# Performance work log

Measured on AMD Instinct MI355X. Metric: run time of the kernel, lower is better.

Reference implementation:

```python
import jax, jax.numpy as jnp
import numpy as np
from jax import lax

IN_CH, FEAT, EMB, P = 384, 256, 32, 64
OUT_CH = (256, 512, 1024, 1024)
EPS_BN = 1e-5


def _conv(x, w, b, stride=1, pad=1, groups=1):
    # x: (B,C,H,W), w: (O, C//groups, kh, kw) torch OIHW layout
    y = lax.conv_general_dilated(x, w, (stride, stride), ((pad, pad), (pad, pad)),
                                 dimension_numbers=('NCHW', 'OIHW', 'NCHW'),
                                 feature_group_count=groups)
    return y + b[None, :, None, None]


def _bn(x, g, b, m, v):
    scale = (g / jnp.sqrt(v + EPS_BN))[None, :, None, None]
    return (x - m[None, :, None, None]) * scale + b[None, :, None, None]


def _convT_block(x, w, b, k):
    # ConvTranspose2d with kernel_size == stride == k, padding 0 (non-overlapping)
    # w: (C_in, C_out, k, k) torch layout
    B, C, H, W = x.shape
    O = w.shape[1]
    y = jnp.einsum('bchw,coij->bohiwj', x, w).reshape(B, O, H * k, W * k)
    return y + b[None, :, None, None]


def _resize_ac(x, oh, ow):
    # bilinear interpolation, align_corners=True; x: (B,C,H,W)
    H, W = x.shape[-2], x.shape[-1]
    def idx(n_in, n_out):
        c = jnp.arange(n_out, dtype=x.dtype) * ((n_in - 1) / max(n_out - 1, 1))
        i0 = jnp.clip(jnp.floor(c).astype(jnp.int32), 0, max(n_in - 2, 0))
        return i0, c - i0.astype(x.dtype)
    if oh != H:
        i0, t = idx(H, oh)
        x = x[:, :, i0, :] * (1.0 - t)[:, None] + x[:, :, jnp.minimum(i0 + 1, H - 1), :] * t[:, None]
    if ow != W:
        j0, t = idx(W, ow)
        x = x[:, :, :, j0] * (1.0 - t) + x[:, :, :, jnp.minimum(j0 + 1, W - 1)] * t
    return x


def _avg3(x):
    # F.avg_pool2d(k=3, s=1, p=1) with count_include_pad=True -> always /9
    s = lax.reduce_window(x, jnp.float32(0.0), lax.add, (1, 1, 3, 3), (1, 1, 1, 1),
                          ((0, 0), (0, 0), (1, 1), (1, 1)))
    return s / 9.0


def _forward(tokens0, tokens1, tokens2, tokens3,
             proj_w0, proj_b0, proj_w1, proj_b1, proj_w2, proj_b2, proj_w3, proj_b3,
             up_w0, up_b0, up_w1, up_b1, down_w3, down_b3,
             fuse_w, fuse_b,
             pe_w1, pe_b1, pe_bn_g, pe_bn_b, pe_bn_m, pe_bn_v, pe_w2, pe_b2,
             prototypes, prototype_biases, bias_scale,
             smooth_w, smooth_b,
             head_w1, head_b1, hbn1_g, hbn1_b, hbn1_m, hbn1_v,
             head_w2, head_b2, hbn2_g, hbn2_b, hbn2_m, hbn2_v,
             head_w3, head_b3, residual_scale,
             patch_h, patch_w):
    B = tokens0.shape[0]
    toks = (tokens0, tokens1, tokens2, tokens3)
    proj = ((proj_w0, proj_b0), (proj_w1, proj_b1), (proj_w2, proj_b2), (proj_w3, proj_b3))
    feats = []
    for t, (w, b) in zip(toks, proj):
        x = t.transpose(0, 2, 1).reshape(B, t.shape[-1], patch_h, patch_w)
        x = jnp.einsum('bchw,oc->bohw', x, w[:, :, 0, 0]) + b[None, :, None, None]  # 1x1 proj
        feats.append(x)
    f0 = _convT_block(feats[0], up_w0, up_b0, 4)
    f1 = _convT_block(feats[1], up_w1, up_b1, 2)
    f2 = feats[2]                                         # identity
    f3 = _conv(feats[3], down_w3, down_b3, stride=2)
    th, tw = f0.shape[-2], f0.shape[-1]
    fused = jnp.concatenate([f0, _resize_ac(f1, th, tw), _resize_ac(f2, th, tw), _resize_ac(f3, th, tw)], axis=1)
    path1 = jax.nn.relu(jnp.einsum('bchw,oc->bohw', fused, fuse_w[:, :, 0, 0]) + fuse_b[None, :, None, None])
    H, W = patch_h * 14, patch_w * 14
    path1 = _resize_ac(path1, H, W)
    pe = _conv(path1, pe_w1, pe_b1)
    pe = jax.nn.relu(_bn(pe, pe_bn_g, pe_bn_b, pe_bn_m, pe_bn_v))
    pe = _conv(pe, pe_w2, pe_b2)                          # (B, EMB, H, W)
    sim = jnp.einsum('behw,pe->bphw', pe, prototypes) / jnp.sqrt(jnp.float32(pe.shape[1]))
    # edge map from embedding gradients, replicate-padded
    gx = jnp.abs(pe[:, :, :, :-1] - pe[:, :, :, 1:])
    gy = jnp.abs(pe[:, :, :-1, :] - pe[:, :, 1:, :])
    gx = jnp.concatenate([gx, gx[:, :, :, -1:]], axis=3)
    gy = jnp.concatenate([gy, gy[:, :, -1:, :]], axis=2)
    edge = (gx.mean(axis=1, keepdims=True) + gy.mean(axis=1, keepdims=True)) * 0.5
    mask = (edge > edge.mean()).astype(pe.dtype)
    for _ in range(2):  # fixed 2-step edge-aware smoothing
        sim = mask * sim + (1.0 - mask) * _avg3(sim)
    # first softmax over prototypes -> entropy regularizer
    act1 = jax.nn.softmax(sim, axis=1)
    activation_entropy = -(act1 * jnp.log(act1 + 1e-8)).sum(axis=1).mean()
    # spatial smoothing conv then second softmax over prototypes
    sim = _conv(sim, smooth_w, smooth_b)
    act = jax.nn.softmax(sim, axis=1)                     # (B, P, H, W)
    bb = 1.0 + jnp.tanh(prototype_biases) * bias_scale    # (P,)
    base_biases = jnp.broadcast_to(bb[None, :], (B, bb.shape[0]))
    base_gain = jnp.einsum('bphw,p->bhw', act, bb)[:, None]  # (B,1,H,W)
    # 64 per-prototype residual heads == grouped convs with groups=P
    n_proto = act.shape[1]
    h = jax.nn.relu(_bn(_conv(act, head_w1, head_b1, groups=n_proto), hbn1_g, hbn1_b, hbn1_m, hbn1_v))
    h = jax.nn.relu(_bn(_conv(h, head_w2, head_b2, groups=n_proto), hbn2_g, hbn2_b, hbn2_m, hbn2_v))
    res = _conv(h, head_w3, head_b3, groups=n_proto)      # (B, P, H, W)
    weighted = (act * res).sum(axis=1, keepdims=True)
    gain = base_gain * (1.0 + jnp.tanh(weighted) * residual_scale)
    instance_bias_map = jnp.clip(gain, 0.5, 2.0)
    return instance_bias_map, act, base_biases, weighted, pe, activation_entropy


def setup_inputs() -> dict:
    key = jax.random.key(0)
    B, N, PH, PW = 2, 256, 16, 16
    ks = iter(jax.random.split(key, 48))
    def rnd(shape, s=1.0):
        return jax.random.normal(next(ks), shape, dtype=jnp.float32) * s
    inp = {}
    for i in range(4):
        inp['tokens%d' % i] = rnd((B, N, IN_CH))
    for i, oc in enumerate(OUT_CH):
        inp['proj_w%d' % i] = rnd((oc, IN_CH, 1, 1), 0.02)
        inp['proj_b%d' % i] = rnd((oc,), 0.01)
    inp['up_w0'] = rnd((OUT_CH[0], OUT_CH[0], 4, 4), 0.02)
    inp['up_b0'] = rnd((OUT_CH[0],), 0.01)
    inp['up_w1'] = rnd((OUT_CH[1], OUT_CH[1], 2, 2), 0.02)
    inp['up_b1'] = rnd((OUT_CH[1],), 0.01)
    inp['down_w3'] = rnd((OUT_CH[3], OUT_CH[3], 3, 3), 0.01)
    inp['down_b3'] = rnd((OUT_CH[3],), 0.01)
    inp['fuse_w'] = rnd((FEAT, sum(OUT_CH), 1, 1), 0.01)
    inp['fuse_b'] = rnd((FEAT,), 0.01)
    inp['pe_w1'] = rnd((FEAT // 2, FEAT, 3, 3), 0.02)
    inp['pe_b1'] = rnd((FEAT // 2,), 0.01)
    inp['pe_bn_g'] = 1.0 + rnd((FEAT // 2,), 0.1)
    inp['pe_bn_b'] = rnd((FEAT // 2,), 0.01)
    inp['pe_bn_m'] = rnd((FEAT // 2,), 0.01)
    inp['pe_bn_v'] = jnp.ones((FEAT // 2,), jnp.float32)
    inp['pe_w2'] = rnd((EMB, FEAT // 2, 3, 3), 0.02)
    inp['pe_b2'] = rnd((EMB,), 0.01)
    inp['prototypes'] = rnd((P, EMB), 0.01)
    inp['prototype_biases'] = rnd((P,), 0.1)
    inp['bias_scale'] = jnp.asarray(0.2, jnp.float32)
    inp['smooth_w'] = rnd((P, P, 3, 3), 0.02)
    inp['smooth_b'] = rnd((P,), 0.01)
    inp['head_w1'] = rnd((P * 8, 1, 3, 3), 0.1)
    inp['head_b1'] = rnd((P * 8,), 0.01)
    inp['hbn1_g'] = 1.0 + rnd((P * 8,), 0.1)
    inp['hbn1_b'] = rnd((P * 8,), 0.01)
    inp['hbn1_m'] = rnd((P * 8,), 0.01)
    inp['hbn1_v'] = jnp.ones((P * 8,), jnp.float32)
    inp['head_w2'] = rnd((P * 8, 8, 3, 3), 0.1)
    inp['head_b2'] = rnd((P * 8,), 0.01)
    inp['hbn2_g'] = 1.0 + rnd((P * 8,), 0.1)
    inp['hbn2_b'] = rnd((P * 8,), 0.01)
    inp['hbn2_m'] = rnd((P * 8,), 0.01)
    inp['hbn2_v'] = jnp.ones((P * 8,), jnp.float32)
    inp['head_w3'] = rnd((P, 8, 3, 3), 0.1)
    inp['head_b3'] = rnd((P,), 0.01)
    inp['residual_scale'] = jnp.asarray(0.1, jnp.float32)
    inp['patch_h'] = PH
    inp['patch_w'] = PW
    return inp


def reference(tokens0, tokens1, tokens2, tokens3,
              proj_w0, proj_b0, proj_w1, proj_b1, proj_w2, proj_b2, proj_w3, proj_b3,
              up_w0, up_b0, up_w1, up_b1, down_w3, down_b3,
              fuse_w, fuse_b,
              pe_w1, pe_b1, pe_bn_g, pe_bn_b, pe_bn_m, pe_bn_v, pe_w2, pe_b2,
              prototypes, prototype_biases, bias_scale,
              smooth_w, smooth_b,
              head_w1, head_b1, hbn1_g, hbn1_b, hbn1_m, hbn1_v,
              head_w2, head_b2, hbn2_g, hbn2_b, hbn2_m, hbn2_v,
              head_w3, head_b3, residual_scale,
              patch_h, patch_w):
    return _forward(tokens0, tokens1, tokens2, tokens3,
                    proj_w0, proj_b0, proj_w1, proj_b1, proj_w2, proj_b2, proj_w3, proj_b3,
                    up_w0, up_b0, up_w1, up_b1, down_w3, down_b3,
                    fuse_w, fuse_b,
                    pe_w1, pe_b1, pe_bn_g, pe_bn_b, pe_bn_m, pe_bn_v, pe_w2, pe_b2,
                    prototypes, prototype_biases, bias_scale,
                    smooth_w, smooth_b,
                    head_w1, head_b1, hbn1_g, hbn1_b, hbn1_m, hbn1_v,
                    head_w2, head_b2, hbn2_g, hbn2_b, hbn2_m, hbn2_v,
                    head_w3, head_b3, residual_scale,
                    patch_h, patch_w)
```

## Files before the change

kernel.cpp:

```cpp
#include <hip/hip_runtime.h>
#include <math.h>

#define BATCH 2
#define NTOK 256
#define INCH 384
#define NP 50176
#define HW 224
#define NPROTO 64
#define EMBD 32

#define OFF_FEATS0   0u
#define OFF_FEATS1   131072u
#define OFF_FEATS2   393216u
#define OFF_FEATS3   917504u
#define OFF_TOKT     1441792u
#define OFF_F0       2228224u
#define OFF_F1       4325376u
#define OFF_F3       5373952u
#define OFF_FUSEDBF  5505024u
#define OFF_WD       5505024u
#define OFF_PART     14942208u
#define OFF_P64C     28573696u
#define OFF_P224C    0u
#define OFF_T1       25690112u
#define OFF_SIMA     0u
#define OFF_SIMB     6422528u
#define OFF_EDGE     12845056u
#define OFF_RES      13000000u
#define OFF_WB       13000000u
#define OFF_SHIFT    13200000u
#define OFF_BGAIN    19422528u
#define OFF_BB       19522880u
#define OFF_ACC      19523008u
#define OFF_WF       19523072u
#define OFF_WFUSE    20000000u
#define OFF_WCV0     20500000u
#define OFF_WCV1     21600000u
#define OFF_WC2      22700000u
#define OFF_WSM      22750000u

#define O_IBM 0u
#define O_ACT 100352u
#define O_BB  6522880u
#define O_WT  6523008u
#define O_PE  6623360u
#define O_ENT 9834624u

typedef __attribute__((ext_vector_type(8))) short bf16x8;
typedef __attribute__((ext_vector_type(4))) float f32x4;
typedef __attribute__((ext_vector_type(2))) float f32x2;

__device__ __forceinline__ short f2bf(float f) {
    unsigned u = __float_as_uint(f);
    unsigned r = (u + 0x7fffu + ((u >> 16) & 1u)) >> 16;
    return (short)r;
}
__device__ __forceinline__ float bf2f(short s) {
    return __uint_as_float(((unsigned)(unsigned short)s) << 16);
}

__global__ void k_transpose(const float* __restrict__ in, float* __restrict__ out) {
    int idx = blockIdx.x * 256 + threadIdx.x;
    int n = idx & 255;
    int c = (idx >> 8) % INCH;
    int b = idx / (INCH * NTOK);
    out[idx] = in[(size_t)b * INCH * NTOK + (size_t)n * INCH + c];
}

__global__ __launch_bounds__(256) void k_proj(const float* __restrict__ A,
                                              const float* __restrict__ W,
                                              const float* __restrict__ bias,
                                              float* __restrict__ out, int O) {
    int p = threadIdx.x;
    int o = blockIdx.x, b = blockIdx.y;
    const float* a = A + (size_t)b * INCH * NTOK + p;
    const float* w = W + (size_t)o * INCH;
    float acc = bias[o];
    for (int c = 0; c < INCH; ++c) acc = fmaf(a[(size_t)c * NTOK], w[c], acc);
    out[((size_t)b * O + o) * NTOK + p] = acc;
}

template <int NT>
__global__ __launch_bounds__(256) void k_wcvprep(const float* __restrict__ W,
                                                 float* __restrict__ WP, int C, int M) {
    __shared__ float t[32][33];
    int c0 = blockIdx.x * 32, m0 = blockIdx.y * 32;
    int tx = threadIdx.x & 31, ty = threadIdx.x >> 5;
#pragma unroll
    for (int r = 0; r < 4; ++r) {
        int cl = ty + r * 8;
        t[cl][tx] = W[(size_t)(c0 + cl) * M + m0 + tx];
    }
    __syncthreads();
    for (int i = threadIdx.x; i < 1024; i += 256) {
        int ml = i % NT;
        int tmp = i / NT;
        int cl = tmp & 31;
        int mh = tmp >> 5;
        WP[(size_t)(m0 / NT + mh) * C * NT + (size_t)(c0 + cl) * NT + ml] = t[cl][mh * NT + ml];
    }
}

template <int NT, int CCH, int K>
__global__ __launch_bounds__(256) void k_convt2(const float* __restrict__ X,
                                                const float* __restrict__ WP,
                                                const float* __restrict__ bias,
                                                float* __restrict__ out,
                                                int C, int O) {
    __shared__ float sX[CCH * 256];
    int tid = threadIdx.x;
    int nt = blockIdx.x, b = blockIdx.y;
    float acc[NT];
#pragma unroll
    for (int j = 0; j < NT; ++j) acc[j] = 0.f;
    const float* Xb = X + (size_t)b * C * 256;
    for (int cc = 0; cc < C; cc += CCH) {
        __syncthreads();
        const f32x4* Xg4 = (const f32x4*)(Xb + (size_t)cc * 256);
        f32x4* s4 = (f32x4*)sX;
        for (int i = tid; i < CCH * 64; i += 256) s4[i] = Xg4[i];
        __syncthreads();
        const float* wr = WP + ((size_t)nt * C + cc) * NT;
        for (int c = 0; c < CCH; ++c) {
            float xv = sX[c * 256 + tid];
            const float* w = wr + c * NT;
#pragma unroll
            for (int j = 0; j < NT; ++j) acc[j] = fmaf(xv, w[j], acc[j]);
        }
    }
    int h = tid >> 4, w = tid & 15;
    int S = 16 * K;
#pragma unroll
    for (int j = 0; j < NT; ++j) {
        int m = nt * NT + j;
        int o = m / (K * K);
        int ij = m - o * (K * K);
        int ii = ij / K, jj = ij - ii * K;
        out[((size_t)b * O + o) * (size_t)(S * S) + (h * K + ii) * S + (w * K + jj)] =
            acc[j] + bias[o];
    }
}

__global__ __launch_bounds__(256) void k_wdprep(const float* __restrict__ W,
                                                float* __restrict__ WP) {
    __shared__ float t[32][33];
    int k0 = blockIdx.x * 32, o0 = blockIdx.y * 32;
    int tx = threadIdx.x & 31, ty = threadIdx.x >> 5;
#pragma unroll
    for (int r = 0; r < 4; ++r) {
        int orow = ty + r * 8;
        t[orow][tx] = W[(size_t)(o0 + orow) * 9216 + k0 + tx];
    }
    __syncthreads();
#pragma unroll
    for (int r = 0; r < 4; ++r) {
        int krow = ty + r * 8;
        int o = o0 + tx;
        WP[(size_t)(o >> 6) * 589824 + (size_t)(k0 + krow) * 64 + (o & 63)] = t[tx][krow];
    }
}

__global__ __launch_bounds__(256) void k_down2(const float* __restrict__ X,
                                               const float* __restrict__ WP,
                                               float* __restrict__ part) {
    __shared__ float sX[64 * 256];
    int tid = threadIdx.x;
    int ot = blockIdx.x, kc = blockIdx.y, b = blockIdx.z;
    int c0 = kc * 64;
    const float* Xg = X + ((size_t)b * 1024 + c0) * 256;
    for (int i = tid; i < 16384; i += 256) {
        int c = i >> 8, px = i & 255;
        int sy = px >> 4, sx = px & 15;
        int par = (sy & 1) * 2 + (sx & 1);
        sX[(c * 4 + par) * 64 + (sy >> 1) * 8 + (sx >> 1)] = Xg[i];
    }
    __syncthreads();
    int lane = tid & 63;
    int w = __builtin_amdgcn_readfirstlane(tid >> 6);
    int oh = lane >> 3, ow = lane & 7;
    int loff[9]; float lmsk[9];
#pragma unroll
    for (int kh = 0; kh < 3; ++kh)
#pragma unroll
        for (int kw = 0; kw < 3; ++kw) {
            int py = (kh == 1) ? 0 : 1;
            int pxp = (kw == 1) ? 0 : 1;
            int u = oh - ((kh == 0) ? 1 : 0);
            int v = ow - ((kw == 0) ? 1 : 0);
            float m = (u >= 0 && v >= 0) ? 1.f : 0.f;
            if (u < 0) u = 0;
            if (v < 0) v = 0;
            loff[kh * 3 + kw] = (py * 2 + pxp) * 64 + u * 8 + v;
            lmsk[kh * 3 + kw] = m;
        }
    float acc[16];
#pragma unroll
    for (int j = 0; j < 16; ++j) acc[j] = 0.f;
    const float* wb = WP + (size_t)ot * 589824 + (size_t)c0 * 576 + w * 16;
    for (int c = 0; c < 64; ++c) {
        const float* xb = sX + c * 256;
        const float* wc = wb + (size_t)c * 576;
#pragma unroll
        for (int tap = 0; tap < 9; ++tap) {
            float xv = xb[loff[tap]] * lmsk[tap];
            const float* wr = wc + tap * 64;
#pragma unroll
            for (int j = 0; j < 16; ++j) acc[j] = fmaf(xv, wr[j], acc[j]);
        }
    }
    float* pp = part + ((size_t)((kc * 2 + b) * 1024 + ot * 64 + w * 16)) * 64 + lane;
#pragma unroll
    for (int j = 0; j < 16; ++j) pp[(size_t)j * 64] = acc[j];
}

__global__ __launch_bounds__(256) void k_downred(const float* __restrict__ part,
                                                 const float* __restrict__ bias,
                                                 float* __restrict__ out) {
    int idx = blockIdx.x * 256 + threadIdx.x;
    int o = (idx >> 6) & 1023;
    int b = idx >> 16;
    int px = idx & 63;
    float s = bias[o];
#pragma unroll
    for (int kcs = 0; kcs < 16; ++kcs)
        s += part[((size_t)(kcs * 2 + b) * 1024 + o) * 64 + px];
    out[idx] = s;
}

__global__ void k_fusedcat_bf(const float* __restrict__ f0, const float* __restrict__ f1,
                              const float* __restrict__ f2, const float* __restrict__ f3,
                              short* __restrict__ out) {
    int idx = blockIdx.x * 256 + threadIdx.x;
    int ch = idx % 2816;
    int t = idx / 2816;
    int pos = t & 4095;
    int b = t >> 12;
    float v;
    if (ch < 256) {
        v = f0[((size_t)(b * 256 + ch)) * 4096 + pos];
    } else {
        const float* src; int sh;
        if (ch < 768)       { src = f1 + ((size_t)(b * 512 + (ch - 256))) * 1024; sh = 32; }
        else if (ch < 1792) { src = f2 + ((size_t)(b * 1024 + (ch - 768))) * 256; sh = 16; }
        else                { src = f3 + ((size_t)(b * 1024 + (ch - 1792))) * 64; sh = 8;  }
        int y = pos >> 6, x = pos & 63;
        float r = (float)(sh - 1) / 63.0f;
        float cy = y * r, cx = x * r;
        int i0 = (int)cy; if (i0 > sh - 2) i0 = sh - 2;
        int j0 = (int)cx; if (j0 > sh - 2) j0 = sh - 2;
        float ty = cy - (float)i0, tx = cx - (float)j0;
        const float* s0 = src + i0 * sh + j0;
        float v00 = s0[0], v01 = s0[1], v10 = s0[sh], v11 = s0[sh + 1];
        float c0 = v00 + ty * (v10 - v00);
        float c1 = v01 + ty * (v11 - v01);
        v = c0 + tx * (c1 - c0);
    }
    out[idx] = f2bf(v);
}

__global__ void k_wfuseprep(const float* __restrict__ w, short* __restrict__ wb) {
    int idx = blockIdx.x * 256 + threadIdx.x;
    int j = idx & 7;
    int lane = (idx >> 3) & 63;
    int ntile = (idx >> 9) & 15;
    int chunk = idx >> 13;
    int oc = ntile * 16 + (lane & 15);
    int c = chunk * 32 + (lane >> 4) * 8 + j;
    wb[idx] = f2bf(w[(size_t)oc * 2816 + c]);
}

__global__ __launch_bounds__(256) void k_fuse_mfma(const short* __restrict__ A,
                                                   const bf16x8* __restrict__ WB,
                                                   const float* __restrict__ bias,
                                                   short* __restrict__ out) {
    int tid = threadIdx.x;
    int lane = tid & 63, w = tid >> 6;
    int row0 = blockIdx.x * 16;
    int l15 = lane & 15, q = lane >> 4;
    int arow = row0 + l15;
    f32x4 acc[4];
#pragma unroll
    for (int nn = 0; nn < 4; ++nn) acc[nn] = (f32x4){0.f, 0.f, 0.f, 0.f};
    const short* arp = A + (size_t)arow * 2816 + q * 8;
    for (int chunk = 0; chunk < 88; ++chunk) {
        bf16x8 a = *(const bf16x8*)(arp + chunk * 32);
        const bf16x8* wbp = WB + ((size_t)(chunk * 16 + w * 4) * 64) + lane;
#pragma unroll
        for (int nn = 0; nn < 4; ++nn) {
            bf16x8 bf = wbp[nn * 64];
            acc[nn] = __builtin_amdgcn_mfma_f32_16x16x32_bf16(a, bf, acc[nn], 0, 0, 0);
        }
    }
#pragma unroll
    for (int nn = 0; nn < 4; ++nn) {
        int oc = (w * 4 + nn) * 16 + l15;
        float bs = bias[oc];
#pragma unroll
        for (int r = 0; r < 4; ++r) {
            int m = q * 4 + r;
            out[(size_t)(row0 + m) * 256 + oc] = f2bf(fmaxf(acc[nn][r] + bs, 0.f));
        }
    }
}

__global__ void k_resize224bf2(const short* __restrict__ in, short* __restrict__ out) {
    int idx = blockIdx.x * 256 + threadIdx.x;
    int c8 = (idx & 31) * 8;
    int p = idx >> 5;
    int b = p / NP;
    int pos = p - b * NP;
    int y = pos / HW, x = pos - y * HW;
    const float r = (float)(63.0 / 223.0);
    float cy = y * r, cx = x * r;
    int i0 = (int)cy; if (i0 > 62) i0 = 62;
    int j0 = (int)cx; if (j0 > 62) j0 = 62;
    float ty = cy - (float)i0, tx = cx - (float)j0;
    const short* base = in + ((size_t)b * 4096) * 256 + c8;
    const bf16x8 v00 = *(const bf16x8*)(base + (size_t)(i0 * 64 + j0) * 256);
    const bf16x8 v01 = *(const bf16x8*)(base + (size_t)(i0 * 64 + j0 + 1) * 256);
    const bf16x8 v10 = *(const bf16x8*)(base + (size_t)((i0 + 1) * 64 + j0) * 256);
    const bf16x8 v11 = *(const bf16x8*)(base + (size_t)((i0 + 1) * 64 + j0 + 1) * 256);
    bf16x8 o;
#pragma unroll
    for (int k = 0; k < 8; ++k) {
        float a00 = bf2f(v00[k]), a01 = bf2f(v01[k]);
        float a10 = bf2f(v10[k]), a11 = bf2f(v11[k]);
        float c0 = a00 + ty * (a10 - a00);
        float c1 = a01 + ty * (a11 - a01);
        o[k] = f2bf(c0 + tx * (c1 - c0));
    }
    *(bf16x8*)(out + ((size_t)b * NP + pos) * 256 + c8) = o;
}

__global__ void k_w1prep(const float* __restrict__ w, const float* __restrict__ bias,
                         const float* __restrict__ g, const float* __restrict__ bb,
                         const float* __restrict__ m, const float* __restrict__ v,
                         short* __restrict__ wb, float* __restrict__ shift) {
    int idx = blockIdx.x * 256 + threadIdx.x;
    int j = idx & 7;
    int lane = (idx >> 3) & 63;
    int nt = (idx >> 9) & 7;
    int tc = idx >> 12;
    int tap = tc % 9, chunk = tc / 9;
    int oc = nt * 16 + (lane & 15);
    int c = chunk * 32 + (lane >> 4) * 8 + j;
    float s = g[oc] * rsqrtf(v[oc] + 1e-5f);
    wb[idx] = f2bf(w[((size_t)oc * 256 + c) * 9 + tap] * s);
    if (idx < 128) {
        float si = g[idx] * rsqrtf(v[idx] + 1e-5f);
        shift[idx] = (bias[idx] - m[idx]) * si + bb[idx];
    }
}

__global__ __launch_bounds__(256) void k_conv1mfma(const short* __restrict__ X,
                                                   const bf16x8* __restrict__ WB,
                                                   const float* __restrict__ shift,
                                                   float* __restrict__ out) {
    int tid = threadIdx.x;
    int lane = tid & 63, w = tid >> 6;
    int t = blockIdx.x;
    int b = blockIdx.y;
    int ty0 = (t / 28) * 16, tx0 = (t % 28) * 8;
    int l15 = lane & 15, q = lane >> 4;
    int loc0 = w * 32 + l15;
    int loc1 = loc0 + 16;
    int py0 = ty0 + (loc0 >> 3), px0 = tx0 + (loc0 & 7);
    int py1 = ty0 + (loc1 >> 3), px1 = tx0 + (loc1 & 7);
    int csub = q * 8;
    f32x4 acc0[8], acc1[8];
#pragma unroll
    for (int nt = 0; nt < 8; ++nt) {
        acc0[nt] = (f32x4){0.f, 0.f, 0.f, 0.f};
        acc1[nt] = (f32x4){0.f, 0.f, 0.f, 0.f};
    }
    const short* Xb = X + (size_t)b * NP * 256;
    const bf16x8 zv = {0, 0, 0, 0, 0, 0, 0, 0};
    for (int chunk = 0; chunk < 8; ++chunk) {
        int c0 = chunk * 32 + csub;
#pragma unroll
        for (int tap = 0; tap < 9; ++tap) {
            int dy = tap / 3 - 1, dx = tap % 3 - 1;
            int sy0 = py0 + dy, sx0 = px0 + dx;
            int sy1 = py1 + dy, sx1 = px1 + dx;
            bf16x8 a0 = zv, a1 = zv;
            if ((unsigned)sy0 < HW && (unsigned)sx0 < HW)
                a0 = *(const bf16x8*)(Xb + ((size_t)sy0 * HW + sx0) * 256 + c0);
            if ((unsigned)sy1 < HW && (unsigned)sx1 < HW)
                a1 = *(const bf16x8*)(Xb + ((size_t)sy1 * HW + sx1) * 256 + c0);
            const bf16x8* wbp = WB + (size_t)((chunk * 9 + tap) * 8) * 64 + lane;
#pragma unroll
            for (int nt = 0; nt < 8; ++nt) {
                bf16x8 bf = wbp[nt * 64];
                acc0[nt] = __builtin_amdgcn_mfma_f32_16x16x32_bf16(a0, bf, acc0[nt], 0, 0, 0);
                acc1[nt] = __builtin_amdgcn_mfma_f32_16x16x32_bf16(a1, bf, acc1[nt], 0, 0, 0);
            }
        }
    }
    int m0 = w * 32, m1 = w * 32 + 16;
#pragma unroll
    for (int nt = 0; nt < 8; ++nt) {
        int oc = nt * 16 + l15;
        float sh = shift[oc];
        float* ob = out + ((size_t)(b * 128 + oc)) * NP;
#pragma unroll
        for (int r = 0; r < 4; ++r) {
            int md = q * 4 + r;
            int lm = m0 + md;
            int py = ty0 + (lm >> 3), px = tx0 + (lm & 7);
            ob[py * HW + px] = fmaxf(acc0[nt][r] + sh, 0.f);
            lm = m1 + md;
            py = ty0 + (lm >> 3); px = tx0 + (lm & 7);
            ob[py * HW + px] = fmaxf(acc1[nt][r] + sh, 0.f);
        }
    }
}

__global__ void k_wc3prep(const float* __restrict__ W, float* __restrict__ WP,
                          int C, int O) {
    int idx = blockIdx.x * 256 + threadIdx.x;
    if (idx >= C * 9 * O) return;
    int o = idx % O;
    int t = idx / O;
    int tap = t % 9, c = t / 9;
    WP[idx] = W[((size_t)o * C + c) * 9 + tap];
}

template <int O, int C, int CCH>
__global__ __launch_bounds__(256) void k_conv3v2(const float* __restrict__ in,
                                                 const float* __restrict__ WP,
                                                 const float* __restrict__ bias,
                                                 float* __restrict__ out) {
    __shared__ float sX[CCH * 324];
    int tid = threadIdx.x;
    int tb = blockIdx.x, b = blockIdx.y;
    int ty0 = (tb / 14) * 16, tx0 = (tb % 14) * 16;
    int px = tid & 15, py = tid >> 4;
    float acc[O];
#pragma unroll
    for (int o = 0; o < O; ++o) acc[o] = 0.f;
    const float* ic = in + (size_t)b * C * NP;
    for (int cc = 0; cc < C; cc += CCH) {
        __syncthreads();
        for (int i = tid; i < CCH * 324; i += 256) {
            int c = i / 324;
            int r = i - c * 324;
            int y = r / 18, x = r - y * 18;
            int sy = ty0 + y - 1, sx = tx0 + x - 1;
            float v = 0.f;
            if ((unsigned)sy < HW && (unsigned)sx < HW)
                v = ic[(size_t)(cc + c) * NP + sy * HW + sx];
            sX[i] = v;
        }
        __syncthreads();
        const float* wr = WP + (size_t)cc * 9 * O;
        const float* xb = sX + py * 18 + px;
#pragma unroll 1
        for (int c = 0; c < CCH; ++c) {
            const float* xc = xb + c * 324;
            const float* wc = wr + (size_t)c * 9 * O;
#pragma unroll
            for (int kh = 0; kh < 3; ++kh)
#pragma unroll
                for (int kw = 0; kw < 3; ++kw) {
                    float xv = xc[kh * 18 + kw];
                    const float* wt = wc + (kh * 3 + kw) * O;
#pragma unroll
                    for (int o = 0; o < O; ++o) acc[o] = fmaf(xv, wt[o], acc[o]);
                }
        }
    }
    int gy = ty0 + py, gx = tx0 + px;
    float* ob = out + (size_t)b * O * NP + (size_t)gy * HW + gx;
#pragma unroll
    for (int o = 0; o < O; ++o) ob[(size_t)o * NP] = acc[o] + bias[o];
}

__global__ __launch_bounds__(256) void k_sim(const float* __restrict__ pe,
                                             const float* __restrict__ proto,
                                             float* __restrict__ sim) {
    int idx = blockIdx.x * 256 + threadIdx.x;
    int b = idx / NP, pos = idx - b * NP;
    const float* p = pe + (size_t)b * EMBD * NP + pos;
    float v[EMBD];
#pragma unroll
    for (int e = 0; e < EMBD; ++e) v[e] = p[(size_t)e * NP];
    const float scale = 1.0f / sqrtf(32.0f);
    float* so = sim + (size_t)b * NPROTO * NP + pos;
    for (int q = 0; q < NPROTO; ++q) {
        float acc = 0.f;
#pragma unroll
        for (int e = 0; e < EMBD; ++e) acc = fmaf(v[e], proto[q * EMBD + e], acc);
        so[(size_t)q * NP] = acc * scale;
    }
}

__global__ void k_init(float* acc) { if (threadIdx.x < 8) acc[threadIdx.x] = 0.f; }

__device__ __forceinline__ float block_reduce_sum(float v) {
    __shared__ float sh[4];
#pragma unroll
    for (int off = 32; off > 0; off >>= 1) v += __shfl_down(v, off);
    int lane = threadIdx.x & 63, wv = threadIdx.x >> 6;
    if (lane == 0) sh[wv] = v;
    __syncthreads();
    return (threadIdx.x == 0) ? (sh[0] + sh[1] + sh[2] + sh[3]) : 0.f;
}

__global__ __launch_bounds__(256) void k_edge(const float* __restrict__ pe,
                                              float* __restrict__ edge,
                                              float* __restrict__ acc) {
    int idx = blockIdx.x * 256 + threadIdx.x;
    int b = idx / NP, pos = idx - b * NP;
    int h = pos / HW, w = pos - h * HW;
    int wn = (w < HW - 1) ? w : HW - 2;
    int hn = (h < HW - 1) ? h : HW - 2;
    const float* pb = pe + (size_t)b * EMBD * NP;
    float sx = 0.f, sy = 0.f;
#pragma unroll 4
    for (int e = 0; e < EMBD; ++e) {
        const float* p = pb + (size_t)e * NP;
        sx += fabsf(p[h * HW + wn] - p[h * HW + wn + 1]);
        sy += fabsf(p[hn * HW + w] - p[hn * HW + HW + w]);
    }
    float ev = (sx + sy) * (0.5f / 32.0f);
    edge[idx] = ev;
    float tot = block_reduce_sum(ev);
    if (threadIdx.x == 0) atomicAdd(acc, tot);
}

__global__ void k_smooth(const float* __restrict__ sin_, const float* __restrict__ edge,
                         const float* __restrict__ acc, float* __restrict__ sout) {
    int idx = blockIdx.x * 256 + threadIdx.x;
    int pos = idx % NP;
    int bp = idx / NP;
    int b = bp >> 6;
    int h = pos / HW, w = pos - h * HW;
    float mean = acc[0] * (1.0f / 100352.0f);
    float m = (edge[(size_t)b * NP + pos] > mean) ? 1.f : 0.f;
    const float* sc = sin_ + (size_t)bp * NP;
    float s = 0.f;
#pragma unroll
    for (int dy = -1; dy <= 1; ++dy) {
        int yy = h + dy;
        if (yy < 0 || yy >= HW) continue;
#pragma unroll
        for (int dx = -1; dx <= 1; ++dx) {
            int xx = w + dx;
            if (xx < 0 || xx >= HW) continue;
            s += sc[yy * HW + xx];
        }
    }
    float c = sc[pos];
    sout[idx] = m * c + (1.f - m) * (s * (1.0f / 9.0f));
}

__global__ __launch_bounds__(256) void k_entropy(const float* __restrict__ sim,
                                                 float* __restrict__ acc) {
    int idx = blockIdx.x * 256 + threadIdx.x;
    int b = idx / NP, pos = idx - b * NP;
    const float* s = sim + (size_t)b * NPROTO * NP + pos;
    float v[NPROTO];
    float mx = -3.0e38f;
#pragma unroll
    for (int q = 0; q < NPROTO; ++q) { v[q] = s[(size_t)q * NP]; mx = fmaxf(mx, v[q]); }
    float sum = 0.f;
#pragma unroll
    for (int q = 0; q < NPROTO; ++q) { float e = expf(v[q] - mx); v[q] = e; sum += e; }
    float inv = 1.f / sum;
    float ent = 0.f;
#pragma unroll
    for (int q = 0; q < NPROTO; ++q) {
        float a = v[q] * inv;
        ent -= a * logf(a + 1e-8f);
    }
    float tot = block_reduce_sum(ent);
    if (threadIdx.x == 0) atomicAdd(acc + 1, tot);
}

__global__ void k_bb(const float* __restrict__ pb, const float* __restrict__ bs,
                     float* __restrict__ bbuf, float* __restrict__ obb) {
    int t = threadIdx.x;
    if (t < NPROTO) {
        float v = 1.f + tanhf(pb[t]) * bs[0];
        bbuf[t] = v;
        obb[t] = v;
        obb[NPROTO + t] = v;
    }
}

__global__ __launch_bounds__(256) void k_actsm(const float* __restrict__ sim,
                                               const float* __restrict__ bb,
                                               float* __restrict__ act,
                                               float* __restrict__ bgain) {
    int idx = blockIdx.x * 256 + threadIdx.x;
    int b = idx / NP, pos = idx - b * NP;
    const float* s = sim + (size_t)b * NPROTO * NP + pos;
    float v[NPROTO];
    float mx = -3.0e38f;
#pragma unroll
    for (int q = 0; q < NPROTO; ++q) { v[q] = s[(size_t)q * NP]; mx = fmaxf(mx, v[q]); }
    float sum = 0.f;
#pragma unroll
    for (int q = 0; q < NPROTO; ++q) { float e = expf(v[q] - mx); v[q] = e; sum += e; }
    float inv = 1.f / sum;
    float* a = act + (size_t)b * NPROTO * NP + pos;
    float bg = 0.f;
#pragma unroll
    for (int q = 0; q < NPROTO; ++q) {
        float p = v[q] * inv;
        a[(size_t)q * NP] = p;
        bg = fmaf(p, bb[q], bg);
    }
    bgain[idx] = bg;
}

__global__ void k_headprep(const float* __restrict__ w1, const float* __restrict__ b1,
                           const float* __restrict__ g1, const float* __restrict__ be1,
                           const float* __restrict__ m1, const float* __restrict__ v1,
                           const float* __restrict__ w2, const float* __restrict__ b2,
                           const float* __restrict__ g2, const float* __restrict__ be2,
                           const float* __restrict__ m2, const float* __restrict__ v2,
                           float* __restrict__ wf) {
    int oc = blockIdx.x * 256 + threadIdx.x;
    if (oc >= 512) return;
    float s1 = g1[oc] * rsqrtf(v1[oc] + 1e-5f);
#pragma unroll
    for (int k = 0; k < 9; ++k) wf[oc * 9 + k] = w1[oc * 9 + k] * s1;
    wf[41472 + oc] = (b1[oc] - m1[oc]) * s1 + be1[oc];
    float s2 = g2[oc] * rsqrtf(v2[oc] + 1e-5f);
    int g = oc >> 3, j = oc & 7;
#pragma unroll
    for (int icc = 0; icc < 8; ++icc)
#pragma unroll
        for (int k = 0; k < 9; ++k)
            wf[4608 + (size_t)g * 576 + icc * 72 + j * 9 + k] = w2[((size_t)oc * 8 + icc) * 9 + k] * s2;
    wf[41984 + oc] = (b2[oc] - m2[oc]) * s2 + be2[oc];
}

__global__ __launch_bounds__(256) void k_heads(
    const float* __restrict__ act, const float* __restrict__ wf,
    const float* __restrict__ w3, const float* __restrict__ b3,
    float* __restrict__ res) {
    __shared__ float sA[22 * 24];
    __shared__ float sH1[8][20 * 22];
    __shared__ float sH2[8][18 * 18];
    int tid = threadIdx.x;
    int tile = blockIdx.x, g = blockIdx.y, b = blockIdx.z;
    int oy0 = (tile / 14) * 16, ox0 = (tile % 14) * 16;
    const float* ain = act + (size_t)(b * NPROTO + g) * NP;

    for (int i = tid; i < 484; i += 256) {
        int y = i / 22, x = i - y * 22;
        int gy = oy0 - 3 + y, gx = ox0 - 3 + x;
        float v = 0.f;
        if ((unsigned)gy < HW && (unsigned)gx < HW) v = ain[gy * HW + gx];
        sA[y * 24 + x] = v;
    }
    __syncthreads();

    const float* b1f = wf + 41472 + g * 8;
    for (int i = tid; i < 400; i += 256) {
        int y = i / 20, x = i - y * 20;
        int gy = oy0 - 2 + y, gx = ox0 - 2 + x;
        float keep = ((unsigned)gy < HW && (unsigned)gx < HW) ? 1.f : 0.f;
        const float* s0 = sA + y * 24 + x;
        float r0 = s0[0],  r1 = s0[1],  r2 = s0[2];
        float r3 = s0[24], r4 = s0[25], r5 = s0[26];
        float r6 = s0[48], r7 = s0[49], r8 = s0[50];
#pragma unroll
        for (int j = 0; j < 8; ++j) {
            const float* w = wf + (g * 8 + j) * 9;
            float v = fmaf(r0, w[0], fmaf(r1, w[1], fmaf(r2, w[2],
                      fmaf(r3, w[3], fmaf(r4, w[4], fmaf(r5, w[5],
                      fmaf(r6, w[6], fmaf(r7, w[7], fmaf(r8, w[8], b1f[j])))))))));
            sH1[j][y * 22 + x] = fmaxf(v, 0.f) * keep;
        }
    }
    __syncthreads();

    const float* w2f = wf + 4608 + (size_t)g * 576;
    const float* b2f = wf + 41984 + g * 8;
    if (tid < 162) {
        int y2 = tid / 9, xp = (tid - y2 * 9) * 2;
        f32x2 a2[8];
#pragma unroll
        for (int j = 0; j < 8; ++j) { float bv = b2f[j]; a2[j] = (f32x2){bv, bv}; }
#pragma unroll
        for (int icc = 0; icc < 8; ++icc) {
            const float* s0 = &sH1[icc][y2 * 22 + xp];
            f32x2 t[9];
#pragma unroll
            for (int r = 0; r < 3; ++r) {
                float f0 = s0[r * 22], f1 = s0[r * 22 + 1];
                float f2 = s0[r * 22 + 2], f3 = s0[r * 22 + 3];
                t[r * 3 + 0] = (f32x2){f0, f1};
                t[r * 3 + 1] = (f32x2){f1, f2};
                t[r * 3 + 2] = (f32x2){f2, f3};
            }
            const float* wr = w2f + icc * 72;
#pragma unroll
            for (int j = 0; j < 8; ++j) {
                const float* wj = wr + j * 9;
#pragma unroll
                for (int k = 0; k < 9; ++k) {
                    float wv = wj[k];
                    a2[j] = __builtin_elementwise_fma(t[k], (f32x2){wv, wv}, a2[j]);
                }
            }
        }
        int gy = oy0 - 1 + y2;
        int gx0 = ox0 - 1 + xp;
        float k0 = ((unsigned)gy < HW && (unsigned)gx0 < HW) ? 1.f : 0.f;
        float k1 = ((unsigned)gy < HW && (unsigned)(gx0 + 1) < HW) ? 1.f : 0.f;
        f32x2 kp = (f32x2){k0, k1};
        const f32x2 z2 = (f32x2){0.f, 0.f};
#pragma unroll
        for (int j = 0; j < 8; ++j) {
            f32x2 v = __builtin_elementwise_max(a2[j], z2) * kp;
            sH2[j][y2 * 18 + xp] = v.x;
            sH2[j][y2 * 18 + xp + 1] = v.y;
        }
    }
    __syncthreads();

    if (tid < 128) {
        int y3 = tid >> 3, xp = (tid & 7) * 2;
        float bv = b3[g];
        f32x2 a2 = (f32x2){bv, bv};
#pragma unroll
        for (int icc = 0; icc < 8; ++icc) {
            const float* s0 = &sH2[icc][y3 * 18 + xp];
            const float* w = w3 + (size_t)(g * 8 + icc) * 9;
#pragma unroll
            for (int r = 0; r < 3; ++r) {
                float f0 = s0[r * 18], f1 = s0[r * 18 + 1];
                float f2 = s0[r * 18 + 2], f3 = s0[r * 18 + 3];
                float w0 = w[r * 3], w1 = w[r * 3 + 1], w2v = w[r * 3 + 2];
                a2 = __builtin_elementwise_fma((f32x2){f0, f1}, (f32x2){w0, w0}, a2);
                a2 = __builtin_elementwise_fma((f32x2){f1, f2}, (f32x2){w1, w1}, a2);
                a2 = __builtin_elementwise_fma((f32x2){f2, f3}, (f32x2){w2v, w2v}, a2);
            }
        }
        float* rp = res + (size_t)(b * NPROTO + g) * NP + (size_t)(oy0 + y3) * HW + (ox0 + xp);
        rp[0] = a2.x;
        rp[1] = a2.y;
    }
}

__global__ __launch_bounds__(256) void k_final(const float* __restrict__ act,
                                               const float* __restrict__ res,
                                               const float* __restrict__ bgain,
                                               const float* __restrict__ rscale,
                                               float* __restrict__ owt,
                                               float* __restrict__ oibm) {
    int idx = blockIdx.x * 256 + threadIdx.x;
    int b = idx / NP, pos = idx - b * NP;
    const float* a = act + (size_t)b * NPROTO * NP + pos;
    const float* r = res + (size_t)b * NPROTO * NP + pos;
    float wt = 0.f;
#pragma unroll
    for (int q = 0; q < NPROTO; ++q) wt = fmaf(a[(size_t)q * NP], r[(size_t)q * NP], wt);
    owt[idx] = wt;
    float gn = bgain[idx] * (1.f + tanhf(wt) * rscale[0]);
    gn = fminf(fmaxf(gn, 0.5f), 2.0f);
    oibm[idx] = gn;
}

__global__ void k_entfinal(const float* __restrict__ acc, float* __restrict__ o) {
    if (threadIdx.x == 0) o[0] = acc[1] * (1.0f / 100352.0f);
}

extern "C" void kernel_launch(void* const* d_in, const int* in_sizes, int n_in,
                              void* d_out, int out_size, void* d_ws, size_t ws_size,
                              hipStream_t stream) {
    const float* tokens[4] = {(const float*)d_in[0], (const float*)d_in[1],
                              (const float*)d_in[2], (const float*)d_in[3]};
    const float* proj_w[4] = {(const float*)d_in[4], (const float*)d_in[6],
                              (const float*)d_in[8], (const float*)d_in[10]};
    const float* proj_b[4] = {(const float*)d_in[5], (const float*)d_in[7],
                              (const float*)d_in[9], (const float*)d_in[11]};
    const float* up_w0 = (const float*)d_in[12]; const float* up_b0 = (const float*)d_in[13];
    const float* up_w1 = (const float*)d_in[14]; const float* up_b1 = (const float*)d_in[15];
    const float* down_w3 = (const float*)d_in[16]; const float* down_b3 = (const float*)d_in[17];
    const float* fuse_w = (const float*)d_in[18]; const float* fuse_b = (const float*)d_in[19];
    const float* pe_w1 = (const float*)d_in[20]; const float* pe_b1 = (const float*)d_in[21];
    const float* pe_bn_g = (const float*)d_in[22]; const float* pe_bn_b = (const float*)d_in[23];
    const float* pe_bn_m = (const float*)d_in[24]; const float* pe_bn_v = (const float*)d_in[25];
    const float* pe_w2 = (const float*)d_in[26]; const float* pe_b2 = (const float*)d_in[27];
    const float* prototypes = (const float*)d_in[28];
    const float* proto_biases = (const float*)d_in[29];
    const float* bias_scale = (const float*)d_in[30];
    const float* smooth_w = (const float*)d_in[31]; const float* smooth_b = (const float*)d_in[32];
    const float* hw1 = (const float*)d_in[33]; const float* hb1 = (const float*)d_in[34];
    const float* hg1 = (const float*)d_in[35]; const float* hbe1 = (const float*)d_in[36];
    const float* hm1 = (const float*)d_in[37]; const float* hv1 = (const float*)d_in[38];
    const float* hw2 = (const float*)d_in[39]; const float* hb2 = (const float*)d_in[40];
    const float* hg2 = (const float*)d_in[41]; const float* hbe2 = (const float*)d_in[42];
    const float* hm2 = (const float*)d_in[43]; const float* hv2 = (const float*)d_in[44];
    const float* hw3 = (const float*)d_in[45]; const float* hb3 = (const float*)d_in[46];
    const float* rscale = (const float*)d_in[47];
    (void)in_sizes; (void)n_in; (void)out_size; (void)ws_size;

    float* ws = (float*)d_ws;
    float* FEATS[4] = {ws + OFF_FEATS0, ws + OFF_FEATS1, ws + OFF_FEATS2, ws + OFF_FEATS3};
    float* TOKT = ws + OFF_TOKT;
    float* F0 = ws + OFF_F0; float* F1 = ws + OFF_F1; float* F3 = ws + OFF_F3;
    short* FUSEDBF = (short*)(ws + OFF_FUSEDBF);
    short* P64C = (short*)(ws + OFF_P64C);
    short* P224C = (short*)(ws + OFF_P224C);
    short* WB = (short*)(ws + OFF_WB);
    short* WFUSE = (short*)(ws + OFF_WFUSE);
    float* SHIFT = ws + OFF_SHIFT;
    float* T1 = ws + OFF_T1;
    float* SIMA = ws + OFF_SIMA; float* SIMB = ws + OFF_SIMB;
    float* EDGE = ws + OFF_EDGE; float* RES = ws + OFF_RES;
    float* BGAIN = ws + OFF_BGAIN; float* BBUF = ws + OFF_BB; float* ACC = ws + OFF_ACC;
    float* WF = ws + OFF_WF;
    float* WDP = ws + OFF_WD;
    float* PART = ws + OFF_PART;
    float* WCV0 = ws + OFF_WCV0;
    float* WCV1 = ws + OFF_WCV1;
    float* WC2 = ws + OFF_WC2;
    float* WSM = ws + OFF_WSM;

    float* out = (float*)d_out;
    float* o_ibm = out + O_IBM; float* o_act = out + O_ACT; float* o_bb = out + O_BB;
    float* o_wt = out + O_WT; float* o_pe = out + O_PE; float* o_ent = out + O_ENT;

    const int OCH[4] = {256, 512, 1024, 1024};
    for (int s = 0; s < 4; ++s)
        k_transpose<<<768, 256, 0, stream>>>(tokens[s], TOKT + s * 196608);
    for (int s = 0; s < 4; ++s)
        k_proj<<<dim3(OCH[s], BATCH), 256, 0, stream>>>(TOKT + s * 196608, proj_w[s], proj_b[s],
                                                        FEATS[s], OCH[s]);
    k_wcvprep<16><<<dim3(8, 128), 256, 0, stream>>>(up_w0, WCV0, 256, 4096);
    k_wcvprep<8><<<dim3(16, 64), 256, 0, stream>>>(up_w1, WCV1, 512, 2048);
    k_convt2<16, 64, 4><<<dim3(256, BATCH), 256, 0, stream>>>(FEATS[0], WCV0, up_b0, F0, 256, 256);
    k_convt2<8, 64, 2><<<dim3(256, BATCH), 256, 0, stream>>>(FEATS[1], WCV1, up_b1, F1, 512, 512);
    k_wdprep<<<dim3(288, 32), 256, 0, stream>>>(down_w3, WDP);
    k_down2<<<dim3(16, 16, BATCH), 256, 0, stream>>>(FEATS[3], WDP, PART);
    k_downred<<<512, 256, 0, stream>>>(PART, down_b3, F3);
    k_wc3prep<<<144, 256, 0, stream>>>(pe_w2, WC2, 128, 32);
    k_wc3prep<<<144, 256, 0, stream>>>(smooth_w, WSM, 64, 64);
    k_wfuseprep<<<2816, 256, 0, stream>>>(fuse_w, WFUSE);
    k_fusedcat_bf<<<90112, 256, 0, stream>>>(F0, F1, FEATS[2], F3, FUSEDBF);
    k_fuse_mfma<<<512, 256, 0, stream>>>(FUSEDBF, (const bf16x8*)WFUSE, fuse_b, P64C);
    k_w1prep<<<1152, 256, 0, stream>>>(pe_w1, pe_b1, pe_bn_g, pe_bn_b, pe_bn_m, pe_bn_v,
                                       WB, SHIFT);
    k_resize224bf2<<<12544, 256, 0, stream>>>(P64C, P224C);
    k_conv1mfma<<<dim3(392, BATCH), 256, 0, stream>>>(P224C, (const bf16x8*)WB, SHIFT, T1);
    k_conv3v2<32, 128, 16><<<dim3(196, BATCH), 256, 0, stream>>>(T1, WC2, pe_b2, o_pe);
    k_sim<<<392, 256, 0, stream>>>(o_pe, prototypes, SIMA);
    k_init<<<1, 64, 0, stream>>>(ACC);
    k_edge<<<392, 256, 0, stream>>>(o_pe, EDGE, ACC);
    k_smooth<<<25088, 256, 0, stream>>>(SIMA, EDGE, ACC, SIMB);
    k_smooth<<<25088, 256, 0, stream>>>(SIMB, EDGE, ACC, SIMA);
    k_entropy<<<392, 256, 0, stream>>>(SIMA, ACC);
    k_conv3v2<64, 64, 16><<<dim3(196, BATCH), 256, 0, stream>>>(SIMA, WSM, smooth_b, SIMB);
    k_bb<<<1, 64, 0, stream>>>(proto_biases, bias_scale, BBUF, o_bb);
    k_actsm<<<392, 256, 0, stream>>>(SIMB, BBUF, o_act, BGAIN);
    k_headprep<<<2, 256, 0, stream>>>(hw1, hb1, hg1, hbe1, hm1, hv1,
                                      hw2, hb2, hg2, hbe2, hm2, hv2, WF);
    k_heads<<<dim3(196, 64, BATCH), 256, 0, stream>>>(o_act, WF, hw3, hb3, RES);
    k_final<<<392, 256, 0, stream>>>(o_act, RES, BGAIN, rscale, o_wt, o_ibm);
    k_entfinal<<<1, 1, 0, stream>>>(ACC, o_ent);
}
```

Before: 1.793 ms.

## Split 3x3 conv input channels across blocks with a separate reduction kernel

The direct 3x3 convolution kernel now splits the input channels into chunks handled by separate blocks (split-K), which multiplies the grid size from 392 to 1568 or 784 blocks and should raise occupancy on the GPU. Each block writes partial sums to a workspace, and a new reduction kernel adds the partials and the bias. The spatial tile changes from 16x16 to 8x32 with a padded shared-memory row stride. The cost is extra global traffic for the partial buffers, one extra launch per conv, and new workspace regions that reuse offsets which must not overlap live data.

```diff
diff --git a/kernel.cpp b/kernel.cpp
--- a/kernel.cpp
+++ b/kernel.cpp
@@ -23,6 +23,8 @@
 #define OFF_P64C     28573696u
 #define OFF_P224C    0u
 #define OFF_T1       25690112u
+#define OFF_PC2      0u
+#define OFF_PSM      25690112u
 #define OFF_SIMA     0u
 #define OFF_SIMB     6422528u
 #define OFF_EDGE     12845056u
@@ -425,44 +427,44 @@
     WP[idx] = W[((size_t)o * C + c) * 9 + tap];
 }
 
-template <int O, int C, int CCH>
-__global__ __launch_bounds__(256) void k_conv3v2(const float* __restrict__ in,
+template <int O, int CB>
+__global__ __launch_bounds__(256) void k_conv3v3(const float* __restrict__ in,
                                                  const float* __restrict__ WP,
-                                                 const float* __restrict__ bias,
-                                                 float* __restrict__ out) {
-    __shared__ float sX[CCH * 324];
+                                                 float* __restrict__ part, int C) {
+    __shared__ float sX[8 * 360];
     int tid = threadIdx.x;
-    int tb = blockIdx.x, b = blockIdx.y;
-    int ty0 = (tb / 14) * 16, tx0 = (tb % 14) * 16;
-    int px = tid & 15, py = tid >> 4;
+    int tb = blockIdx.x, s = blockIdx.y, b = blockIdx.z;
+    int ty0 = (tb / 7) * 8, tx0 = (tb % 7) * 32;
+    int px = tid & 31, py = tid >> 5;
     float acc[O];
 #pragma unroll
     for (int o = 0; o < O; ++o) acc[o] = 0.f;
-    const float* ic = in + (size_t)b * C * NP;
-    for (int cc = 0; cc < C; cc += CCH) {
+    int c0 = s * CB;
+    const float* ic = in + ((size_t)b * C + c0) * NP;
+    const float* wbase = WP + (size_t)c0 * 9 * O;
+    for (int cc = 0; cc < CB; cc += 8) {
         __syncthreads();
-        for (int i = tid; i < CCH * 324; i += 256) {
-            int c = i / 324;
-            int r = i - c * 324;
-            int y = r / 18, x = r - y * 18;
+        for (int i = tid; i < 8 * 340; i += 256) {
+            int c = i / 340;
+            int r = i - c * 340;
+            int y = r / 34, x = r - y * 34;
             int sy = ty0 + y - 1, sx = tx0 + x - 1;
             float v = 0.f;
             if ((unsigned)sy < HW && (unsigned)sx < HW)
                 v = ic[(size_t)(cc + c) * NP + sy * HW + sx];
-            sX[i] = v;
+            sX[c * 360 + y * 36 + x] = v;
         }
         __syncthreads();
-        const float* wr = WP + (size_t)cc * 9 * O;
-        const float* xb = sX + py * 18 + px;
+        const float* xb = sX + py * 36 + px;
 #pragma unroll 1
-        for (int c = 0; c < CCH; ++c) {
-            const float* xc = xb + c * 324;
-            const float* wc = wr + (size_t)c * 9 * O;
+        for (int c = 0; c < 8; ++c) {
+            const float* xc = xb + c * 360;
+            const float* wc = wbase + (size_t)(cc + c) * 9 * O;
 #pragma unroll
             for (int kh = 0; kh < 3; ++kh)
 #pragma unroll
                 for (int kw = 0; kw < 3; ++kw) {
-                    float xv = xc[kh * 18 + kw];
+                    float xv = xc[kh * 36 + kw];
                     const float* wt = wc + (kh * 3 + kw) * O;
 #pragma unroll
                     for (int o = 0; o < O; ++o) acc[o] = fmaf(xv, wt[o], acc[o]);
@@ -470,9 +472,22 @@
         }
     }
     int gy = ty0 + py, gx = tx0 + px;
-    float* ob = out + (size_t)b * O * NP + (size_t)gy * HW + gx;
-#pragma unroll
-    for (int o = 0; o < O; ++o) ob[(size_t)o * NP] = acc[o] + bias[o];
+    float* ob = part + ((size_t)(s * BATCH + b) * O) * NP + (size_t)gy * HW + gx;
+#pragma unroll
+    for (int o = 0; o < O; ++o) ob[(size_t)o * NP] = acc[o];
+}
+
+template <int O, int NS>
+__global__ __launch_bounds__(256) void k_conv3red(const float* __restrict__ part,
+                                                  const float* __restrict__ bias,
+                                                  float* __restrict__ out) {
+    int idx = blockIdx.x * 256 + threadIdx.x;
+    int o = (idx / NP) % O;
+    float v = bias[o];
+#pragma unroll
+    for (int s2 = 0; s2 < NS; ++s2)
+        v += part[(size_t)idx + (size_t)s2 * (BATCH * O * NP)];
+    out[idx] = v;
 }
 
 __global__ __launch_bounds__(256) void k_sim(const float* __restrict__ pe,
@@ -822,6 +837,8 @@
     float* WCV1 = ws + OFF_WCV1;
     float* WC2 = ws + OFF_WC2;
     float* WSM = ws + OFF_WSM;
+    float* PC2 = ws + OFF_PC2;
+    float* PSM = ws + OFF_PSM;
 
     float* out = (float*)d_out;
     float* o_ibm = out + O_IBM; float* o_act = out + O_ACT; float* o_bb = out + O_BB;
@@ -849,14 +866,16 @@
                                        WB, SHIFT);
     k_resize224bf2<<<12544, 256, 0, stream>>>(P64C, P224C);
     k_conv1mfma<<<dim3(392, BATCH), 256, 0, stream>>>(P224C, (const bf16x8*)WB, SHIFT, T1);
-    k_conv3v2<32, 128, 16><<<dim3(196, BATCH), 256, 0, stream>>>(T1, WC2, pe_b2, o_pe);
+    k_conv3v3<32, 32><<<dim3(196, 4, BATCH), 256, 0, stream>>>(T1, WC2, PC2, 128);
+    k_conv3red<32, 4><<<12544, 256, 0, stream>>>(PC2, pe_b2, o_pe);
     k_sim<<<392, 256, 0, stream>>>(o_pe, prototypes, SIMA);
     k_init<<<1, 64, 0, stream>>>(ACC);
     k_edge<<<392, 256, 0, stream>>>(o_pe, EDGE, ACC);
     k_smooth<<<25088, 256, 0, stream>>>(SIMA, EDGE, ACC, SIMB);
     k_smooth<<<25088, 256, 0, stream>>>(SIMB, EDGE, ACC, SIMA);
     k_entropy<<<392, 256, 0, stream>>>(SIMA, ACC);
-    k_conv3v2<64, 64, 16><<<dim3(196, BATCH), 256, 0, stream>>>(SIMA, WSM, smooth_b, SIMB);
+    k_conv3v3<64, 32><<<dim3(196, 2, BATCH), 256, 0, stream>>>(SIMA, WSM, PSM, 64);
+    k_conv3red<64, 2><<<25088, 256, 0, stream>>>(PSM, smooth_b, SIMB);
     k_bb<<<1, 64, 0, stream>>>(proto_biases, bias_scale, BBUF, o_bb);
     k_actsm<<<392, 256, 0, stream>>>(SIMB, BBUF, o_act, BGAIN);
     k_headprep<<<2, 256, 0, stream>>>(hw1, hb1, hg1, hbe1, hm1, hv1,
```

New measurement: 1.582 ms. -11.8%, faster.
